# Optimization experiments

Hardware: AMD Instinct MI355X
Metric: run time of the kernel (lower is better)

The kernel has to match this reference:

```python
import jax, jax.numpy as jnp
import numpy as np

N = 50000          # nodes
E = 400000         # edges (before self loops)
F_IN = 256         # num_node_features
H = 4              # heads
C = 64             # hidden_channels
G = 128            # graphs in batch
NEG_SLOPE = 0.2    # PyG GATConv default


def gat_conv(x, W, att_src, att_dst, bias, src, dst):
    """PyG GATConv (concat=True, add_self_loops=True). x:[N,Fin] -> [N,H*C]."""
    h = (x @ W).reshape(N, H, C)                       # [N,H,C]
    a_src = jnp.einsum('nhc,hc->nh', h, att_src)       # [N,H]
    a_dst = jnp.einsum('nhc,hc->nh', h, att_dst)       # [N,H]
    # add self loops
    loop = jnp.arange(N, dtype=src.dtype)
    s = jnp.concatenate([src, loop])                   # [E+N]
    d = jnp.concatenate([dst, loop])                   # [E+N]
    logits = jax.nn.leaky_relu(a_src[s] + a_dst[d], NEG_SLOPE)  # [E+N,H]
    # segment softmax over destination nodes
    m = jax.ops.segment_max(logits, d, num_segments=N)           # [N,H]
    m = jnp.where(jnp.isneginf(m), 0.0, m)
    ex = jnp.exp(logits - m[d])                                  # [E+N,H]
    denom = jax.ops.segment_sum(ex, d, num_segments=N)           # [N,H]
    alpha = ex / (denom[d] + 1e-16)                              # [E+N,H]
    # weighted scatter-add of source features
    msg = alpha[:, :, None] * h[s]                               # [E+N,H,C]
    out = jax.ops.segment_sum(msg, d, num_segments=N)            # [N,H,C]
    return out.reshape(N, H * C) + bias


def setup_inputs() -> dict:
    key = jax.random.key(0)
    ks = jax.random.split(key, 16)
    HC = H * C
    x = jax.random.normal(ks[0], (N, F_IN), dtype=jnp.float32)
    edge_index = jax.random.randint(ks[1], (2, E), 0, N, dtype=jnp.int32)
    batch = jnp.sort(jax.random.randint(ks[2], (N,), 0, G, dtype=jnp.int32))
    def glorot(k, shape):
        fan = shape[0] + shape[-1]
        return jax.random.uniform(k, shape, jnp.float32, -1.0, 1.0) * np.sqrt(6.0 / fan)
    return {
        'x': x, 'edge_index': edge_index, 'batch': batch,
        'W1': glorot(ks[3], (F_IN, HC)),
        'att_src1': glorot(ks[4], (H, C)), 'att_dst1': glorot(ks[5], (H, C)),
        'b1': jnp.zeros((HC,), jnp.float32),
        'W2': glorot(ks[6], (HC, HC)),
        'att_src2': glorot(ks[7], (H, C)), 'att_dst2': glorot(ks[8], (H, C)),
        'b2': jnp.zeros((HC,), jnp.float32),
        'lin1_w': glorot(ks[9], (HC, HC // 2)), 'lin1_b': jnp.zeros((HC // 2,), jnp.float32),
        'lin2_w': glorot(ks[10], (HC // 2, 2)), 'lin2_b': jnp.zeros((2,), jnp.float32),
    }


def reference(x, edge_index, batch, W1, att_src1, att_dst1, b1,
              W2, att_src2, att_dst2, b2, lin1_w, lin1_b, lin2_w, lin2_b):
    src, dst = edge_index[0], edge_index[1]
    # dropout layers are identity in eval mode
    h = gat_conv(x, W1, att_src1, att_dst1, b1, src, dst)
    h = jax.nn.elu(h)
    h = gat_conv(h, W2, att_src2, att_dst2, b2, src, dst)
    h = jax.nn.elu(h)
    pooled = jax.ops.segment_max(h, batch, num_segments=G)   # [G, H*C]
    pooled = jnp.where(jnp.isneginf(pooled), 0.0, pooled)    # guard empty graphs
    z = pooled @ lin1_w + lin1_b
    z = z @ lin2_w + lin2_b
    return z  # [G, num_classes]
```

## Files before the change

kernel.cpp:

```cpp
#include <hip/hip_runtime.h>
#include <math.h>

#define LRELU_SLOPE 0.2f
#define NEG_INF __int_as_float(0xff800000)

typedef float f32x4 __attribute__((ext_vector_type(4)));
typedef _Float16 f16x8 __attribute__((ext_vector_type(8)));
typedef _Float16 f16x2 __attribute__((ext_vector_type(2)));
typedef unsigned short us8 __attribute__((ext_vector_type(8)));

__device__ __forceinline__ void atomicMaxF(float* addr, float v) {
  if (v >= 0.f) atomicMax((int*)addr, __float_as_int(v));
  else atomicMin((unsigned int*)addr, (unsigned int)__float_as_int(v));
}

__device__ __forceinline__ unsigned short f2h(float f) {
  _Float16 h = (_Float16)f;
  return __builtin_bit_cast(unsigned short, h);
}
__device__ __forceinline__ float2 up2(unsigned int u) {
  f16x2 h = __builtin_bit_cast(f16x2, u);
  return make_float2((float)h.x, (float)h.y);
}

__device__ __forceinline__ void async_copy16(const unsigned short* g, unsigned short* l) {
  __builtin_amdgcn_global_load_lds(
      (const __attribute__((address_space(1))) void*)g,
      (__attribute__((address_space(3))) void*)l, 16, 0, 0);
}

__global__ void conv_w(const float* __restrict__ W1, const float* __restrict__ W2,
                       unsigned short* __restrict__ t1, unsigned short* __restrict__ t2) {
  const float* W = blockIdx.y ? W2 : W1;
  unsigned short* t = blockIdx.y ? t2 : t1;
  int k = blockIdx.x, n = threadIdx.x;
  t[n * 256 + k] = f2h(W[k * 256 + n]);
}

__global__ __launch_bounds__(256) void conv_x(
    const float* __restrict__ x, unsigned short* __restrict__ xo, int total) {
  int base = (blockIdx.x * 256 + threadIdx.x) * 4;
  if (base >= total) return;
  float4 v = *(const float4*)(x + base);
  ushort4 h;
  h.x = f2h(v.x); h.y = f2h(v.y); h.z = f2h(v.z); h.w = f2h(v.w);
  *(ushort4*)(xo + base) = h;
}

__global__ __launch_bounds__(256) void gemm_mfma(
    const unsigned short* __restrict__ A, const unsigned short* __restrict__ Bt,
    const float* __restrict__ att_s, const float* __restrict__ att_d,
    unsigned short* __restrict__ C, float* __restrict__ a_s,
    float* __restrict__ a_d, int M) {
  __shared__ __align__(16) unsigned short sA[128 * 64];
  __shared__ __align__(16) unsigned short sB[128 * 64];
  const int tid = threadIdx.x;
  const int lane = tid & 63;
  const int wave = tid >> 6;
  const int wr = wave >> 1, wc = wave & 1;
  const int bm = blockIdx.x * 128;
  const int bn = blockIdx.y * 128;

  const int srow = lane >> 3;
  const int scol = (((lane & 7) ^ (lane >> 3)) << 3);

  f32x4 acc[4][4];
#pragma unroll
  for (int i = 0; i < 4; ++i)
#pragma unroll
    for (int j = 0; j < 4; ++j) acc[i][j] = (f32x4){0.f, 0.f, 0.f, 0.f};

  for (int kc = 0; kc < 256; kc += 64) {
#pragma unroll
    for (int i = 0; i < 4; ++i) {
      const int r0 = wave * 32 + i * 8;
      const size_t ga = (size_t)(bm + r0 + srow) * 256 + kc + scol;
      const size_t gb = (size_t)(bn + r0 + srow) * 256 + kc + scol;
      async_copy16(A + ga, &sA[r0 * 64]);
      async_copy16(Bt + gb, &sB[r0 * 64]);
    }
    __syncthreads();
#pragma unroll
    for (int ks = 0; ks < 64; ks += 32) {
      const int kbase = ks + ((lane >> 4) << 3);
      const int kx = kbase ^ ((lane & 7) << 3);
      f16x8 af[4], bf[4];
#pragma unroll
      for (int f = 0; f < 4; ++f) {
        int ar = wr * 64 + f * 16 + (lane & 15);
        int br = wc * 64 + f * 16 + (lane & 15);
        af[f] = __builtin_bit_cast(f16x8, *(const us8*)&sA[ar * 64 + kx]);
        bf[f] = __builtin_bit_cast(f16x8, *(const us8*)&sB[br * 64 + kx]);
      }
#pragma unroll
      for (int i = 0; i < 4; ++i)
#pragma unroll
        for (int j = 0; j < 4; ++j)
          acc[i][j] = __builtin_amdgcn_mfma_f32_16x16x32_f16(af[i], bf[j], acc[i][j], 0, 0, 0);
    }
    __syncthreads();
  }

  const int head = blockIdx.y * 2 + wc;
  float ws[4], wd[4];
#pragma unroll
  for (int j = 0; j < 4; ++j) {
    ws[j] = att_s[head * 64 + j * 16 + (lane & 15)];
    wd[j] = att_d[head * 64 + j * 16 + (lane & 15)];
  }
#pragma unroll
  for (int i = 0; i < 4; ++i) {
#pragma unroll
    for (int r = 0; r < 4; ++r) {
      float ps = 0.f, pd = 0.f;
#pragma unroll
      for (int j = 0; j < 4; ++j) {
        ps = fmaf(acc[i][j][r], ws[j], ps);
        pd = fmaf(acc[i][j][r], wd[j], pd);
      }
#pragma unroll
      for (int off = 1; off < 16; off <<= 1) {
        ps += __shfl_xor(ps, off);
        pd += __shfl_xor(pd, off);
      }
      int row = bm + wr * 64 + i * 16 + ((lane >> 4) << 2) + r;
      if ((lane & 15) == 0 && row < M) {
        a_s[row * 4 + head] = ps;
        a_d[row * 4 + head] = pd;
      }
    }
  }

#pragma unroll
  for (int i = 0; i < 4; ++i) {
#pragma unroll
    for (int r = 0; r < 4; ++r) {
      int row = bm + wr * 64 + i * 16 + ((lane >> 4) << 2) + r;
      if (row < M) {
#pragma unroll
        for (int j = 0; j < 4; ++j)
          C[(size_t)row * 256 + bn + wc * 64 + j * 16 + (lane & 15)] = f2h(acc[i][j][r]);
      }
    }
  }
}

__global__ void init_misc(int* __restrict__ count, float* __restrict__ pooled,
                          int N_, int G_) {
  int t = blockIdx.x * 256 + threadIdx.x;
  if (t < N_) count[t] = 1;
  if (t < G_ * 256) pooled[t] = NEG_INF;
}

__global__ void hist_k(const int* __restrict__ dst, int* __restrict__ count, int E_) {
  int t = blockIdx.x * 256 + threadIdx.x;
  if (t < E_) atomicAdd(&count[dst[t]], 1);
}

#define SCB 1024

__global__ __launch_bounds__(256) void scan_phaseA(
    const int* __restrict__ count, int* __restrict__ bsum, int N_) {
  int t = threadIdx.x;
  int base = blockIdx.x * SCB + t * 4;
  int s = 0;
  if (base + 3 < N_) {
    int4 v = *(const int4*)(count + base);
    s = v.x + v.y + v.z + v.w;
  } else {
#pragma unroll
    for (int k = 0; k < 4; ++k) if (base + k < N_) s += count[base + k];
  }
#pragma unroll
  for (int off = 32; off > 0; off >>= 1) s += __shfl_xor(s, off);
  __shared__ int red[4];
  int wave = t >> 6, lane = t & 63;
  if (lane == 0) red[wave] = s;
  __syncthreads();
  if (t == 0) bsum[blockIdx.x] = red[0] + red[1] + red[2] + red[3];
}

__global__ __launch_bounds__(256) void scan_phaseB(
    const int* __restrict__ bsum, int* __restrict__ boff, int nb) {
  __shared__ int tmp[256];
  int t = threadIdx.x;
  int v = (t < nb) ? bsum[t] : 0;
  tmp[t] = v;
  __syncthreads();
  for (int off = 1; off < 256; off <<= 1) {
    int u = (t >= off) ? tmp[t - off] : 0;
    __syncthreads();
    tmp[t] += u;
    __syncthreads();
  }
  if (t < nb) boff[t] = tmp[t] - v;
  if (t == 0) boff[nb] = tmp[255];
}

__global__ __launch_bounds__(256) void scan_phaseC(
    const int* __restrict__ count, const int* __restrict__ boff,
    int* __restrict__ rowptr, int* __restrict__ nxt, int N_, int nb) {
  __shared__ int tmp[256];
  int t = threadIdx.x;
  int base = blockIdx.x * SCB + t * 4;
  int4 v = make_int4(0, 0, 0, 0);
  if (base + 3 < N_) {
    v = *(const int4*)(count + base);
  } else {
    if (base + 0 < N_) v.x = count[base + 0];
    if (base + 1 < N_) v.y = count[base + 1];
    if (base + 2 < N_) v.z = count[base + 2];
  }
  int s = v.x + v.y + v.z + v.w;
  tmp[t] = s;
  __syncthreads();
  for (int off = 1; off < 256; off <<= 1) {
    int u = (t >= off) ? tmp[t - off] : 0;
    __syncthreads();
    tmp[t] += u;
    __syncthreads();
  }
  int run = boff[blockIdx.x] + tmp[t] - s;
  int4 rp;
  rp.x = run; run += v.x;
  rp.y = run; run += v.y;
  rp.z = run; run += v.z;
  rp.w = run;
  if (base + 3 < N_) {
    *(int4*)(rowptr + base) = rp;
    *(int4*)(nxt + base) = rp;
  } else {
    if (base + 0 < N_) { rowptr[base + 0] = rp.x; nxt[base + 0] = rp.x; }
    if (base + 1 < N_) { rowptr[base + 1] = rp.y; nxt[base + 1] = rp.y; }
    if (base + 2 < N_) { rowptr[base + 2] = rp.z; nxt[base + 2] = rp.z; }
  }
  if (blockIdx.x == 0 && t == 0) rowptr[N_] = boff[nb];
}

__global__ void scatter_k(const int* __restrict__ src, const int* __restrict__ dst,
                          int* __restrict__ nxt, int* __restrict__ colx,
                          int* __restrict__ rowx, int E_, int N_) {
  int t = blockIdx.x * 256 + threadIdx.x;
  if (t >= E_ + N_) return;
  int s = (t < E_) ? src[t] : (t - E_);
  int d = (t < E_) ? dst[t] : (t - E_);
  int pos = atomicAdd(&nxt[d], 1);
  colx[pos] = s;
  rowx[pos] = d;
}

__global__ __launch_bounds__(256) void edge_w(
    const int* __restrict__ colx, const int* __restrict__ rowx,
    const float* __restrict__ a_s, const float* __restrict__ a_d,
    float* __restrict__ ew, int T) {
  int t = blockIdx.x * 256 + threadIdx.x;
  if (t >= T) return;
  int s = colx[t], d = rowx[t];
  float4 as4 = *(const float4*)(a_s + (size_t)s * 4);
  float4 ad4 = *(const float4*)(a_d + (size_t)d * 4);
  float l;
  float4 w;
  l = as4.x + ad4.x; l = l > 0.f ? l : LRELU_SLOPE * l; w.x = __expf(l);
  l = as4.y + ad4.y; l = l > 0.f ? l : LRELU_SLOPE * l; w.y = __expf(l);
  l = as4.z + ad4.z; l = l > 0.f ? l : LRELU_SLOPE * l; w.z = __expf(l);
  l = as4.w + ad4.w; l = l > 0.f ? l : LRELU_SLOPE * l; w.w = __expf(l);
  *(float4*)(ew + (size_t)t * 4) = w;
}

__global__ __launch_bounds__(256) void agg(
    const unsigned short* __restrict__ h, const int* __restrict__ rowptr,
    const int* __restrict__ colx, const float* __restrict__ ew,
    const float* __restrict__ bias, unsigned short* __restrict__ out, int N_) {
  const int wave = threadIdx.x >> 6;
  const int lane = threadIdx.x & 63;
  const int n = blockIdx.x * 4 + wave;
  if (n >= N_) return;
  const int head = lane >> 4;
  const size_t coff = (size_t)lane * 4;
  const int e0 = rowptr[n], e1 = rowptr[n + 1];
  float4 acc = make_float4(0.f, 0.f, 0.f, 0.f);
  float dsum = 0.f;
  int j = e0;
  for (; j + 8 <= e1; j += 8) {
    int sx[8];
    float wv[8];
    uint2 gv[8];
#pragma unroll
    for (int u = 0; u < 8; ++u) sx[u] = colx[j + u];
#pragma unroll
    for (int u = 0; u < 8; ++u) wv[u] = ew[(size_t)(j + u) * 4 + head];
#pragma unroll
    for (int u = 0; u < 8; ++u) gv[u] = *(const uint2*)(h + (size_t)sx[u] * 256 + coff);
#pragma unroll
    for (int u = 0; u < 8; ++u) {
      dsum += wv[u];
      float2 a = up2(gv[u].x), b = up2(gv[u].y);
      acc.x = fmaf(wv[u], a.x, acc.x); acc.y = fmaf(wv[u], a.y, acc.y);
      acc.z = fmaf(wv[u], b.x, acc.z); acc.w = fmaf(wv[u], b.y, acc.w);
    }
  }
  for (; j < e1; ++j) {
    int s = colx[j];
    float w = ew[(size_t)j * 4 + head];
    uint2 g = *(const uint2*)(h + (size_t)s * 256 + coff);
    dsum += w;
    float2 a = up2(g.x), b = up2(g.y);
    acc.x = fmaf(w, a.x, acc.x); acc.y = fmaf(w, a.y, acc.y);
    acc.z = fmaf(w, b.x, acc.z); acc.w = fmaf(w, b.y, acc.w);
  }
  const float inv = 1.f / (dsum + 1e-16f);
  const float4 b4 = *(const float4*)(bias + coff);
  float v;
  float4 o;
  v = acc.x * inv + b4.x; o.x = v > 0.f ? v : expm1f(v);
  v = acc.y * inv + b4.y; o.y = v > 0.f ? v : expm1f(v);
  v = acc.z * inv + b4.z; o.z = v > 0.f ? v : expm1f(v);
  v = acc.w * inv + b4.w; o.w = v > 0.f ? v : expm1f(v);
  ushort4 oh;
  oh.x = f2h(o.x); oh.y = f2h(o.y); oh.z = f2h(o.z); oh.w = f2h(o.w);
  *(ushort4*)(out + (size_t)n * 256 + coff) = oh;
}

#define PNB 32
__global__ __launch_bounds__(256) void pool_max(
    const unsigned short* __restrict__ fb, const int* __restrict__ batch,
    float* __restrict__ pooled, int N_) {
  const int c2 = threadIdx.x & 127;
  const int slot = threadIdx.x >> 7;
  const int ns = blockIdx.x * PNB + slot * 16;
  const int ne = min(ns + 16, N_);
  if (ns >= N_) return;
  float r0 = NEG_INF, r1 = NEG_INF;
  int g = batch[ns];
#pragma unroll 4
  for (int n = ns; n < ne; ++n) {
    int gn = batch[n];
    unsigned int w = *(const unsigned int*)(fb + (size_t)n * 256 + c2 * 2);
    if (gn != g) {
      atomicMaxF(&pooled[(size_t)g * 256 + c2 * 2], r0);
      atomicMaxF(&pooled[(size_t)g * 256 + c2 * 2 + 1], r1);
      r0 = r1 = NEG_INF; g = gn;
    }
    float2 xv = up2(w);
    r0 = fmaxf(r0, xv.x);
    r1 = fmaxf(r1, xv.y);
  }
  atomicMaxF(&pooled[(size_t)g * 256 + c2 * 2], r0);
  atomicMaxF(&pooled[(size_t)g * 256 + c2 * 2 + 1], r1);
}

__global__ __launch_bounds__(128) void head_k(
    const float* __restrict__ pooled, const float* __restrict__ w1,
    const float* __restrict__ b1, const float* __restrict__ w2,
    const float* __restrict__ b2, float* __restrict__ out) {
  __shared__ float ps[256];
  __shared__ float z1[128];
  int g = blockIdx.x;
  int t = threadIdx.x;
  for (int i = t; i < 256; i += 128) {
    float v = pooled[(size_t)g * 256 + i];
    if (v < -1e37f) v = 0.f;
    ps[i] = v;
  }
  __syncthreads();
  float a = b1[t];
  for (int k = 0; k < 256; ++k) a = fmaf(ps[k], w1[k * 128 + t], a);
  z1[t] = a;
  __syncthreads();
  if (t < 2) {
    float a2 = b2[t];
    for (int j = 0; j < 128; ++j) a2 = fmaf(z1[j], w2[j * 2 + t], a2);
    out[g * 2 + t] = a2;
  }
}

extern "C" void kernel_launch(void* const* d_in, const int* in_sizes, int n_in,
                              void* d_out, int out_size, void* d_ws, size_t ws_size,
                              hipStream_t stream) {
  const int N = in_sizes[2];
  const int E = in_sizes[1] / 2;
  const int G = out_size / 2;
  const int T = E + N;
  const int Npad = ((N + 127) / 128) * 128;

  const float* x     = (const float*)d_in[0];
  const int*   ei    = (const int*)d_in[1];
  const int*   src   = ei;
  const int*   dst   = ei + E;
  const int*   batch = (const int*)d_in[2];
  const float* W1    = (const float*)d_in[3];
  const float* atts1 = (const float*)d_in[4];
  const float* attd1 = (const float*)d_in[5];
  const float* b1    = (const float*)d_in[6];
  const float* W2    = (const float*)d_in[7];
  const float* atts2 = (const float*)d_in[8];
  const float* attd2 = (const float*)d_in[9];
  const float* b2    = (const float*)d_in[10];
  const float* l1w   = (const float*)d_in[11];
  const float* l1b   = (const float*)d_in[12];
  const float* l2w   = (const float*)d_in[13];
  const float* l2b   = (const float*)d_in[14];

  uintptr_t p = (uintptr_t)d_ws;
  auto alloc = [&](size_t bytes) -> void* {
    p = (p + 255) & ~(uintptr_t)255;
    void* r = (void*)p;
    p += bytes;
    return r;
  };
  const int nb = (N + SCB - 1) / SCB;
  unsigned short* hbuf = (unsigned short*)alloc((size_t)N * 256 * 2);
  unsigned short* xbuf = (unsigned short*)alloc((size_t)Npad * 256 * 2);
  unsigned short* fbuf = (unsigned short*)alloc((size_t)Npad * 256 * 2);
  float* a_s    = (float*)alloc((size_t)N * 4 * 4);
  float* a_d    = (float*)alloc((size_t)N * 4 * 4);
  float* pooled = (float*)alloc((size_t)G * 256 * 4);
  int*   count  = (int*)alloc((size_t)N * 4);
  int*   rowptr = (int*)alloc((size_t)(N + 1) * 4);
  int*   nxt    = (int*)alloc((size_t)N * 4);
  int*   colx   = (int*)alloc((size_t)T * 4);
  int*   rowx   = (int*)alloc((size_t)T * 4);
  float* ew     = (float*)alloc((size_t)T * 4 * 4);
  int*   bsum   = (int*)alloc((size_t)nb * 4);
  int*   boff   = (int*)alloc((size_t)(nb + 1) * 4);
  unsigned short* wt1 = (unsigned short*)alloc(256 * 256 * 2);
  unsigned short* wt2 = (unsigned short*)alloc(256 * 256 * 2);

  dim3 blk(256);
  dim3 gemmGrid(Npad / 128, 2);
  int initRange = max(N, G * 256);
  int xtot = N * 256;

  conv_w<<<dim3(256, 2), blk, 0, stream>>>(W1, W2, wt1, wt2);
  conv_x<<<(xtot / 4 + 255) / 256, blk, 0, stream>>>(x, xbuf, xtot);
  init_misc<<<(initRange + 255) / 256, blk, 0, stream>>>(count, pooled, N, G);
  hist_k<<<(E + 255) / 256, blk, 0, stream>>>(dst, count, E);
  scan_phaseA<<<nb, blk, 0, stream>>>(count, bsum, N);
  scan_phaseB<<<1, blk, 0, stream>>>(bsum, boff, nb);
  scan_phaseC<<<nb, blk, 0, stream>>>(count, boff, rowptr, nxt, N, nb);
  scatter_k<<<(T + 255) / 256, blk, 0, stream>>>(src, dst, nxt, colx, rowx, E, N);

  gemm_mfma<<<gemmGrid, blk, 0, stream>>>(xbuf, wt1, atts1, attd1, hbuf, a_s, a_d, N);
  edge_w<<<(T + 255) / 256, blk, 0, stream>>>(colx, rowx, a_s, a_d, ew, T);
  agg<<<(N + 3) / 4, blk, 0, stream>>>(hbuf, rowptr, colx, ew, b1, fbuf, N);

  gemm_mfma<<<gemmGrid, blk, 0, stream>>>(fbuf, wt2, atts2, attd2, hbuf, a_s, a_d, N);
  edge_w<<<(T + 255) / 256, blk, 0, stream>>>(colx, rowx, a_s, a_d, ew, T);
  agg<<<(N + 3) / 4, blk, 0, stream>>>(hbuf, rowptr, colx, ew, b2, fbuf, N);

  pool_max<<<(N + PNB - 1) / PNB, blk, 0, stream>>>(fbuf, batch, pooled, N);
  head_k<<<G, 128, 0, stream>>>(pooled, l1w, l1b, l2w, l2b, (float*)d_out);
}
```

Measured before the change: 245.4 us.

## Store edge weights head-major and vectorize edge-index and weight loads in aggregation

Edge weights move from an edge-major [T,4] layout to a head-major [4,T] layout, so each head's weights are contiguous. The aggregation loop then fetches four edge indices and four weights per step with single int4/float4 loads, after a scalar prologue that aligns the start to a multiple of four. This is meant to cut the strided per-head weight loads and the count of load instructions. The trade-off is that the inner loop now handles four edges at a time instead of eight, so fewer feature gathers are in flight per wave, and nodes with only a few edges spend more time in the scalar prologue and tail.

```diff
diff --git a/kernel.cpp b/kernel.cpp
--- a/kernel.cpp
+++ b/kernel.cpp
@@ -252,56 +252,67 @@
 __global__ __launch_bounds__(256) void edge_w(
     const int* __restrict__ colx, const int* __restrict__ rowx,
     const float* __restrict__ a_s, const float* __restrict__ a_d,
-    float* __restrict__ ew, int T) {
+    float* __restrict__ ewt, int T) {
   int t = blockIdx.x * 256 + threadIdx.x;
   if (t >= T) return;
   int s = colx[t], d = rowx[t];
   float4 as4 = *(const float4*)(a_s + (size_t)s * 4);
   float4 ad4 = *(const float4*)(a_d + (size_t)d * 4);
   float l;
-  float4 w;
-  l = as4.x + ad4.x; l = l > 0.f ? l : LRELU_SLOPE * l; w.x = __expf(l);
-  l = as4.y + ad4.y; l = l > 0.f ? l : LRELU_SLOPE * l; w.y = __expf(l);
-  l = as4.z + ad4.z; l = l > 0.f ? l : LRELU_SLOPE * l; w.z = __expf(l);
-  l = as4.w + ad4.w; l = l > 0.f ? l : LRELU_SLOPE * l; w.w = __expf(l);
-  *(float4*)(ew + (size_t)t * 4) = w;
+  l = as4.x + ad4.x; l = l > 0.f ? l : LRELU_SLOPE * l; ewt[0 * (size_t)T + t] = __expf(l);
+  l = as4.y + ad4.y; l = l > 0.f ? l : LRELU_SLOPE * l; ewt[1 * (size_t)T + t] = __expf(l);
+  l = as4.z + ad4.z; l = l > 0.f ? l : LRELU_SLOPE * l; ewt[2 * (size_t)T + t] = __expf(l);
+  l = as4.w + ad4.w; l = l > 0.f ? l : LRELU_SLOPE * l; ewt[3 * (size_t)T + t] = __expf(l);
 }
 
 __global__ __launch_bounds__(256) void agg(
     const unsigned short* __restrict__ h, const int* __restrict__ rowptr,
-    const int* __restrict__ colx, const float* __restrict__ ew,
+    const int* __restrict__ colx, const float* __restrict__ ewt, int T,
     const float* __restrict__ bias, unsigned short* __restrict__ out, int N_) {
   const int wave = threadIdx.x >> 6;
   const int lane = threadIdx.x & 63;
   const int n = blockIdx.x * 4 + wave;
   if (n >= N_) return;
   const int head = lane >> 4;
+  const float* ewh = ewt + (size_t)head * T;
   const size_t coff = (size_t)lane * 4;
   const int e0 = rowptr[n], e1 = rowptr[n + 1];
   float4 acc = make_float4(0.f, 0.f, 0.f, 0.f);
   float dsum = 0.f;
   int j = e0;
-  for (; j + 8 <= e1; j += 8) {
-    int sx[8];
-    float wv[8];
-    uint2 gv[8];
-#pragma unroll
-    for (int u = 0; u < 8; ++u) sx[u] = colx[j + u];
-#pragma unroll
-    for (int u = 0; u < 8; ++u) wv[u] = ew[(size_t)(j + u) * 4 + head];
-#pragma unroll
-    for (int u = 0; u < 8; ++u) gv[u] = *(const uint2*)(h + (size_t)sx[u] * 256 + coff);
-#pragma unroll
-    for (int u = 0; u < 8; ++u) {
-      dsum += wv[u];
-      float2 a = up2(gv[u].x), b = up2(gv[u].y);
-      acc.x = fmaf(wv[u], a.x, acc.x); acc.y = fmaf(wv[u], a.y, acc.y);
-      acc.z = fmaf(wv[u], b.x, acc.z); acc.w = fmaf(wv[u], b.y, acc.w);
-    }
+  for (; j < e1 && (j & 3); ++j) {
+    int s = colx[j];
+    float w = ewh[j];
+    uint2 g = *(const uint2*)(h + (size_t)s * 256 + coff);
+    dsum += w;
+    float2 a = up2(g.x), b = up2(g.y);
+    acc.x = fmaf(w, a.x, acc.x); acc.y = fmaf(w, a.y, acc.y);
+    acc.z = fmaf(w, b.x, acc.z); acc.w = fmaf(w, b.y, acc.w);
+  }
+  for (; j + 4 <= e1; j += 4) {
+    int4 s4 = *(const int4*)(colx + j);
+    float4 w4 = *(const float4*)(ewh + j);
+    uint2 g0 = *(const uint2*)(h + (size_t)s4.x * 256 + coff);
+    uint2 g1 = *(const uint2*)(h + (size_t)s4.y * 256 + coff);
+    uint2 g2 = *(const uint2*)(h + (size_t)s4.z * 256 + coff);
+    uint2 g3 = *(const uint2*)(h + (size_t)s4.w * 256 + coff);
+    dsum += (w4.x + w4.y) + (w4.z + w4.w);
+    float2 a0 = up2(g0.x), b0 = up2(g0.y);
+    float2 a1 = up2(g1.x), b1 = up2(g1.y);
+    float2 a2 = up2(g2.x), b2 = up2(g2.y);
+    float2 a3 = up2(g3.x), b3 = up2(g3.y);
+    acc.x = fmaf(w4.x, a0.x, acc.x); acc.y = fmaf(w4.x, a0.y, acc.y);
+    acc.z = fmaf(w4.x, b0.x, acc.z); acc.w = fmaf(w4.x, b0.y, acc.w);
+    acc.x = fmaf(w4.y, a1.x, acc.x); acc.y = fmaf(w4.y, a1.y, acc.y);
+    acc.z = fmaf(w4.y, b1.x, acc.z); acc.w = fmaf(w4.y, b1.y, acc.w);
+    acc.x = fmaf(w4.z, a2.x, acc.x); acc.y = fmaf(w4.z, a2.y, acc.y);
+    acc.z = fmaf(w4.z, b2.x, acc.z); acc.w = fmaf(w4.z, b2.y, acc.w);
+    acc.x = fmaf(w4.w, a3.x, acc.x); acc.y = fmaf(w4.w, a3.y, acc.y);
+    acc.z = fmaf(w4.w, b3.x, acc.z); acc.w = fmaf(w4.w, b3.y, acc.w);
   }
   for (; j < e1; ++j) {
     int s = colx[j];
-    float w = ew[(size_t)j * 4 + head];
+    float w = ewh[j];
     uint2 g = *(const uint2*)(h + (size_t)s * 256 + coff);
     dsum += w;
     float2 a = up2(g.x), b = up2(g.y);
@@ -381,6 +392,7 @@
   const int E = in_sizes[1] / 2;
   const int G = out_size / 2;
   const int T = E + N;
+  const int Tpad = ((T + 3) / 4) * 4;
   const int Npad = ((N + 127) / 128) * 128;
 
   const float* x     = (const float*)d_in[0];
@@ -418,9 +430,9 @@
   int*   count  = (int*)alloc((size_t)N * 4);
   int*   rowptr = (int*)alloc((size_t)(N + 1) * 4);
   int*   nxt    = (int*)alloc((size_t)N * 4);
-  int*   colx   = (int*)alloc((size_t)T * 4);
-  int*   rowx   = (int*)alloc((size_t)T * 4);
-  float* ew     = (float*)alloc((size_t)T * 4 * 4);
+  int*   colx   = (int*)alloc((size_t)Tpad * 4);
+  int*   rowx   = (int*)alloc((size_t)Tpad * 4);
+  float* ewt    = (float*)alloc((size_t)Tpad * 4 * 4);
   int*   bsum   = (int*)alloc((size_t)nb * 4);
   int*   boff   = (int*)alloc((size_t)(nb + 1) * 4);
   unsigned short* wt1 = (unsigned short*)alloc(256 * 256 * 2);
@@ -441,12 +453,12 @@
   scatter_k<<<(T + 255) / 256, blk, 0, stream>>>(src, dst, nxt, colx, rowx, E, N);
 
   gemm_mfma<<<gemmGrid, blk, 0, stream>>>(xbuf, wt1, atts1, attd1, hbuf, a_s, a_d, N);
-  edge_w<<<(T + 255) / 256, blk, 0, stream>>>(colx, rowx, a_s, a_d, ew, T);
-  agg<<<(N + 3) / 4, blk, 0, stream>>>(hbuf, rowptr, colx, ew, b1, fbuf, N);
+  edge_w<<<(T + 255) / 256, blk, 0, stream>>>(colx, rowx, a_s, a_d, ewt, Tpad);
+  agg<<<(N + 3) / 4, blk, 0, stream>>>(hbuf, rowptr, colx, ewt, Tpad, b1, fbuf, N);
 
   gemm_mfma<<<gemmGrid, blk, 0, stream>>>(fbuf, wt2, atts2, attd2, hbuf, a_s, a_d, N);
-  edge_w<<<(T + 255) / 256, blk, 0, stream>>>(colx, rowx, a_s, a_d, ew, T);
-  agg<<<(N + 3) / 4, blk, 0, stream>>>(hbuf, rowptr, colx, ew, b2, fbuf, N);
+  edge_w<<<(T + 255) / 256, blk, 0, stream>>>(colx, rowx, a_s, a_d, ewt, Tpad);
+  agg<<<(N + 3) / 4, blk, 0, stream>>>(hbuf, rowptr, colx, ewt, Tpad, b2, fbuf, N);
 
   pool_max<<<(N + PNB - 1) / PNB, blk, 0, stream>>>(fbuf, batch, pooled, N);
   head_k<<<G, 128, 0, stream>>>(pooled, l1w, l1b, l2w, l2b, (float*)d_out);
```

Measured after the change: 238.9 us. 1.03x faster.
